# Optimization experiments

Measured on AMD Instinct MI355X. Metric: run time of the kernel, lower is better.

The kernel has to match this reference:

```python
import jax, jax.numpy as jnp
import numpy as np

# ---- static config mirroring __init__ kwargs ----
B, GH, GW = 64, 52, 52
A, NC = 5, 80            # anchor_number, class_number
HW = GH * GW
MAXB = 30                # max_box_per_image
NET_W, NET_H = 416.0, 416.0
COORD_SCALE, NOOBJ_SCALE, OBJ_SCALE, CLASS_SCALE = 5.0, 1.0, 5.0, 1.0
OBJ_THRESH = 0.5
ANCHORS_NP = np.array([[10., 14.], [23., 27.], [37., 58.], [81., 82.], [135., 169.]], dtype=np.float32)


def setup_inputs() -> dict:
    key = jax.random.key(0)
    k1, k2, k3, k4, k5, k6, k7, k8 = jax.random.split(key, 8)
    net_out = jax.random.normal(k1, (B, GH, GW, A * (NC + 5)), jnp.float32) * 0.5
    # encoded targets [B, A, 6, HW]: (x_off, y_off, w_log, h_log, conf, class)
    xy = jax.random.uniform(k2, (B, A, 2, HW), jnp.float32)
    whlog = jax.random.normal(k3, (B, A, 2, HW), jnp.float32) * 0.3
    conf = jax.random.uniform(k4, (B, A, 1, HW), jnp.float32)
    cls = jnp.floor(jax.random.uniform(k5, (B, A, 1, HW), jnp.float32) * NC)
    targets = jnp.concatenate([xy, whlog, conf, cls], axis=2)
    anchor_mask = (jax.random.uniform(k6, (B, A, HW), jnp.float32) < 0.02).astype(jnp.float32)
    # GT boxes (x1,y1,x2,y2) in image pixels
    ctr = jax.random.uniform(k7, (B, MAXB, 2), jnp.float32) * NET_W
    sz = jax.random.uniform(k8, (B, MAXB, 2), jnp.float32) * 100.0 + 10.0
    true_bboxs = jnp.concatenate([ctr - sz / 2, ctr + sz / 2], axis=-1)
    anchors = jnp.asarray(ANCHORS_NP)
    return {"net_out": net_out, "targets": targets, "anchor_mask": anchor_mask,
            "true_bboxs": true_bboxs, "anchors": anchors}


def _focal(p, t, gamma=2.0):
    # F.binary_cross_entropy elementwise, then focal modulation
    bce = -(t * jnp.log(p) + (1.0 - t) * jnp.log1p(-p))
    pt = jnp.exp(-bce)
    return (1.0 - pt) ** gamma * bce


def reference(net_out, targets, anchor_mask, true_bboxs, anchors):
    Bs, gh, gw, _ = net_out.shape
    hw = gh * gw
    x = net_out.reshape(Bs, A, NC + 5, hw)
    xy = jax.nn.sigmoid(x[:, :, :2, :])          # [B,A,2,HW]
    wh = x[:, :, 2:4, :]                          # raw w,h logits
    p_conf = jax.nn.sigmoid(x[:, :, 4, :])       # [B,A,HW]

    # ----- class loss (CE over positives) -----
    clas = x[:, :, 5:, :].reshape(Bs * A, NC, hw).transpose(0, 2, 1).reshape(-1, NC)
    clas_mask = anchor_mask.reshape(Bs * A, 1, hw).transpose(0, 2, 1).reshape(-1)
    t_clas = targets[:, :, 5, :].reshape(Bs * A, 1, hw).transpose(0, 2, 1).reshape(-1).astype(jnp.int32)
    logp = jax.nn.log_softmax(clas, axis=-1)
    clas_loss = (-jnp.take_along_axis(logp, t_clas[:, None], axis=1)[:, 0]) * clas_mask

    # ----- coordinate loss (masked, size-weighted MSE) -----
    am = anchor_mask[:, :, None, :]  # [B,A,1,HW]
    wh_scale = 2.0 - targets[:, :, 2:3, :] * targets[:, :, 3:4, :] / (NET_W * NET_H)
    xy_loss = (xy - targets[:, :, 0:2, :]) ** 2 * am * wh_scale
    wh_loss = (wh - targets[:, :, 2:4, :]) ** 2 * am * wh_scale
    coords_loss = xy_loss.sum() + wh_loss.sum()

    # ----- rescale predictions to image-space corner boxes -----
    col = jnp.tile(jnp.arange(gw), gh).astype(jnp.float32)      # [HW]
    row = jnp.repeat(jnp.arange(gh), gw).astype(jnp.float32)    # [HW] (square grid)
    aw = anchors[:, 0][None, :, None]
    ah = anchors[:, 1][None, :, None]
    px = (xy[:, :, 0, :] + col) / gw * NET_W
    py = (xy[:, :, 1, :] + row) / gh * NET_H
    pw = jnp.exp(wh[:, :, 0, :]) * aw
    ph = jnp.exp(wh[:, :, 1, :]) * ah
    x1 = px - pw / 2
    y1 = py - ph / 2
    pred = jnp.stack([x1, y1, x1 + pw, y1 + ph], axis=-1)       # [B,A,HW,4]
    pred = pred.transpose(0, 2, 1, 3)[:, :, :, None, :]         # [B,HW,A,1,4]

    # ----- broadcast IoU vs GT boxes -----
    tb = true_bboxs[:, None, None, :, :]                         # [B,1,1,M,4]
    tl = jnp.maximum(pred[..., :2], tb[..., :2])
    br = jnp.minimum(pred[..., 2:], tb[..., 2:])
    whi = jnp.maximum(br - tl, 0.0)
    inter = whi[..., 0] * whi[..., 1]
    a1 = (pred[..., 2] - pred[..., 0]) * (pred[..., 3] - pred[..., 1])
    a2 = (tb[..., 2] - tb[..., 0]) * (tb[..., 3] - tb[..., 1])
    iou = inter / (a1 + a2 - inter + 1e-5)                       # [B,HW,A,M]
    iou_max = iou.max(axis=-1)                                   # [B,HW,A]

    noobj_mask = 1.0 - anchor_mask
    label_noobj = (iou_max < OBJ_THRESH).astype(jnp.float32).transpose(0, 2, 1) * noobj_mask

    # ----- focal confidence losses -----
    t_conf = targets[:, :, 4, :]
    fl = _focal(p_conf, t_conf)
    obj_conf_loss = (anchor_mask * fl).sum()
    noobj_conf_loss = (label_noobj * fl).sum()

    total = (clas_loss.sum() * CLASS_SCALE
             + coords_loss * COORD_SCALE
             + obj_conf_loss * OBJ_SCALE
             + noobj_conf_loss * NOOBJ_SCALE) / Bs
    return total
```

## Files before the change

kernel.cpp:

```cpp
#include <hip/hip_runtime.h>

#define BATCH   64
#define GH      52
#define GWID    52
#define HW      2704
#define NA      5
#define NC      80
#define MAXB    30
#define CH_STRIDE HW
#define A_STRIDE  (85*HW)
#define B_STRIDE  (NA*85*HW)

__global__ __launch_bounds__(256) void yolo_main(
    const float* __restrict__ net_out,
    const float* __restrict__ targets,
    const float* __restrict__ amask,
    const float* __restrict__ tboxes,
    const float* __restrict__ anchors,
    float* __restrict__ partial)
{
    __shared__ float tb[MAXB * 4];
    __shared__ float wred[4];

    const int ba  = blockIdx.y;
    const int b   = ba / NA;
    const int a   = ba - b * NA;
    const int tid = threadIdx.x;

    if (tid < MAXB * 4) tb[tid] = tboxes[(size_t)b * (MAXB * 4) + tid];
    __syncthreads();

    const int p = blockIdx.x * 256 + tid;
    float local = 0.f;

    if (p < HW) {
        const size_t nb    = (size_t)b * B_STRIDE + (size_t)a * A_STRIDE + p;
        const size_t tbase = ((size_t)(b * NA + a) * 6) * HW + p;

        const float t_x   = targets[tbase];
        const float t_y   = targets[tbase + 1 * HW];
        const float t_w   = targets[tbase + 2 * HW];
        const float t_h   = targets[tbase + 3 * HW];
        const float t_c   = targets[tbase + 4 * HW];
        const int   t_cls = (int)targets[tbase + 5 * HW];

        const float am = amask[(size_t)(b * NA + a) * HW + p];

        const float zx = net_out[nb];
        const float zy = net_out[nb + 1 * CH_STRIDE];
        const float tw = net_out[nb + 2 * CH_STRIDE];
        const float th = net_out[nb + 3 * CH_STRIDE];
        const float zc = net_out[nb + 4 * CH_STRIDE];

        const float sx = 1.f / (1.f + __builtin_expf(-zx));
        const float sy = 1.f / (1.f + __builtin_expf(-zy));
        const float pc = 1.f / (1.f + __builtin_expf(-zc));

        const float ws = 2.f - t_w * t_h * (1.f / (416.f * 416.f));
        const float dx = sx - t_x, dy = sy - t_y, dw = tw - t_w, dh = th - t_h;
        const float coords = (dx * dx + dy * dy + dw * dw + dh * dh) * ws * am;

        const float log_pc   = -__builtin_logf(1.f + __builtin_expf(-zc));
        const float log_1mpc = -__builtin_logf(1.f + __builtin_expf(zc));
        const float bce = -(t_c * log_pc + (1.f - t_c) * log_1mpc);
        const float pt  = __builtin_expf(-bce);
        const float omp = 1.f - pt;
        const float fl  = omp * omp * bce;

        const float aw = anchors[a * 2 + 0];
        const float ah = anchors[a * 2 + 1];
        const float px = (sx + (float)(p % GWID)) * (416.f / (float)GWID);
        const float py = (sy + (float)(p / GWID)) * (416.f / (float)GH);
        const float pw = __builtin_expf(tw) * aw;
        const float ph = __builtin_expf(th) * ah;
        const float x1 = px - pw * 0.5f;
        const float y1 = py - ph * 0.5f;
        const float x2 = x1 + pw;
        const float y2 = y1 + ph;
        const float a1 = (x2 - x1) * (y2 - y1);

        float ioumax = 0.f;
        #pragma unroll
        for (int k = 0; k < MAXB; ++k) {
            const float bx1 = tb[k * 4 + 0];
            const float by1 = tb[k * 4 + 1];
            const float bx2 = tb[k * 4 + 2];
            const float by2 = tb[k * 4 + 3];
            const float tlx = fmaxf(x1, bx1);
            const float tly = fmaxf(y1, by1);
            const float brx = fminf(x2, bx2);
            const float bry = fminf(y2, by2);
            const float wi  = fmaxf(brx - tlx, 0.f);
            const float hi  = fmaxf(bry - tly, 0.f);
            const float inter = wi * hi;
            const float a2  = (bx2 - bx1) * (by2 - by1);
            const float iou = inter / (a1 + a2 - inter + 1e-5f);
            ioumax = fmaxf(ioumax, iou);
        }

        const float noobj = (ioumax < 0.5f) ? (1.f - am) : 0.f;

        local = 5.0f * coords + 5.0f * am * fl + noobj * fl;

        if (am > 0.f) {
            float lg[NC];
            #pragma unroll
            for (int c = 0; c < NC; ++c)
                lg[c] = net_out[nb + (size_t)(5 + c) * CH_STRIDE];
            float m = lg[0];
            #pragma unroll
            for (int c = 1; c < NC; ++c) m = fmaxf(m, lg[c]);
            float s = 0.f;
            #pragma unroll
            for (int c = 0; c < NC; ++c) s += __builtin_expf(lg[c] - m);
            float vt = 0.f;
            #pragma unroll
            for (int c = 0; c < NC; ++c) vt = (c == t_cls) ? lg[c] : vt;
            local += -(vt - m - __builtin_logf(s)) * am;
        }
    }

    #pragma unroll
    for (int off = 32; off > 0; off >>= 1)
        local += __shfl_down(local, off, 64);
    const int wid  = tid >> 6;
    const int lane = tid & 63;
    if (lane == 0) wred[wid] = local;
    __syncthreads();
    if (tid == 0) {
        partial[(size_t)blockIdx.y * gridDim.x + blockIdx.x] =
            wred[0] + wred[1] + wred[2] + wred[3];
    }
}

__global__ __launch_bounds__(256) void yolo_reduce(
    const float* __restrict__ partial, int n, float* __restrict__ out)
{
    __shared__ double sred[4];
    const int tid = threadIdx.x;
    double s = 0.0;
    for (int i = tid; i < n; i += 256) s += (double)partial[i];
    #pragma unroll
    for (int off = 32; off > 0; off >>= 1)
        s += __shfl_down(s, off, 64);
    const int wid  = tid >> 6;
    const int lane = tid & 63;
    if (lane == 0) sred[wid] = s;
    __syncthreads();
    if (tid == 0) {
        const double tot = sred[0] + sred[1] + sred[2] + sred[3];
        out[0] = (float)(tot / (double)BATCH);
    }
}

extern "C" void kernel_launch(void* const* d_in, const int* in_sizes, int n_in,
                              void* d_out, int out_size, void* d_ws, size_t ws_size,
                              hipStream_t stream) {
    const float* net_out = (const float*)d_in[0];
    const float* targets = (const float*)d_in[1];
    const float* amask   = (const float*)d_in[2];
    const float* tboxes  = (const float*)d_in[3];
    const float* anchors = (const float*)d_in[4];
    float* partial = (float*)d_ws;
    float* out = (float*)d_out;

    const int gx = (HW + 255) / 256;
    dim3 grid(gx, BATCH * NA);
    yolo_main<<<grid, 256, 0, stream>>>(net_out, targets, amask, tboxes, anchors, partial);
    yolo_reduce<<<1, 256, 0, stream>>>(partial, gx * BATCH * NA, out);
}
```

Baseline: 405.2 us.

## Compute class cross-entropy cooperatively across the wavefront per positive anchor

Positive anchors are found with a wavefront ballot, and each is handled by all 64 lanes. Each lane loads one or two class logits, and the max and sum-exp are done with xor shuffles, replacing the per-thread serial 80-element gather and loop. This removes divergent, strided per-thread loads and the large register array that could limit occupancy. Out-of-range threads are clamped to a valid pixel instead of branching, so uniform control flow can run the ballot loop. The cost is a serial loop over positives in each wave, with shuffle overhead per positive.

```diff
diff --git a/kernel.cpp b/kernel.cpp
--- a/kernel.cpp
+++ b/kernel.cpp
@@ -26,105 +26,120 @@
     const int b   = ba / NA;
     const int a   = ba - b * NA;
     const int tid = threadIdx.x;
+    const int lane = tid & 63;
 
     if (tid < MAXB * 4) tb[tid] = tboxes[(size_t)b * (MAXB * 4) + tid];
     __syncthreads();
 
-    const int p = blockIdx.x * 256 + tid;
-    float local = 0.f;
+    const int  p_raw = blockIdx.x * 256 + tid;
+    const bool valid = (p_raw < HW);
+    const int  p     = valid ? p_raw : (HW - 1);
 
-    if (p < HW) {
-        const size_t nb    = (size_t)b * B_STRIDE + (size_t)a * A_STRIDE + p;
-        const size_t tbase = ((size_t)(b * NA + a) * 6) * HW + p;
+    const size_t nbase = (size_t)b * B_STRIDE + (size_t)a * A_STRIDE;
+    const size_t nb    = nbase + p;
+    const size_t tbase = ((size_t)ba * 6) * HW + p;
 
-        const float t_x   = targets[tbase];
-        const float t_y   = targets[tbase + 1 * HW];
-        const float t_w   = targets[tbase + 2 * HW];
-        const float t_h   = targets[tbase + 3 * HW];
-        const float t_c   = targets[tbase + 4 * HW];
-        const int   t_cls = (int)targets[tbase + 5 * HW];
+    const float t_x   = targets[tbase];
+    const float t_y   = targets[tbase + 1 * HW];
+    const float t_w   = targets[tbase + 2 * HW];
+    const float t_h   = targets[tbase + 3 * HW];
+    const float t_c   = targets[tbase + 4 * HW];
+    const int   t_cls = (int)targets[tbase + 5 * HW];
 
-        const float am = amask[(size_t)(b * NA + a) * HW + p];
+    float am = amask[(size_t)ba * HW + p];
+    if (!valid) am = 0.f;
 
-        const float zx = net_out[nb];
-        const float zy = net_out[nb + 1 * CH_STRIDE];
-        const float tw = net_out[nb + 2 * CH_STRIDE];
-        const float th = net_out[nb + 3 * CH_STRIDE];
-        const float zc = net_out[nb + 4 * CH_STRIDE];
+    const float zx = net_out[nb];
+    const float zy = net_out[nb + 1 * CH_STRIDE];
+    const float tw = net_out[nb + 2 * CH_STRIDE];
+    const float th = net_out[nb + 3 * CH_STRIDE];
+    const float zc = net_out[nb + 4 * CH_STRIDE];
 
-        const float sx = 1.f / (1.f + __builtin_expf(-zx));
-        const float sy = 1.f / (1.f + __builtin_expf(-zy));
-        const float pc = 1.f / (1.f + __builtin_expf(-zc));
+    const float sx = 1.f / (1.f + __builtin_expf(-zx));
+    const float sy = 1.f / (1.f + __builtin_expf(-zy));
 
-        const float ws = 2.f - t_w * t_h * (1.f / (416.f * 416.f));
-        const float dx = sx - t_x, dy = sy - t_y, dw = tw - t_w, dh = th - t_h;
-        const float coords = (dx * dx + dy * dy + dw * dw + dh * dh) * ws * am;
+    const float ws = 2.f - t_w * t_h * (1.f / (416.f * 416.f));
+    const float dx = sx - t_x, dy = sy - t_y, dw = tw - t_w, dh = th - t_h;
+    const float coords = (dx * dx + dy * dy + dw * dw + dh * dh) * ws * am;
 
-        const float log_pc   = -__builtin_logf(1.f + __builtin_expf(-zc));
-        const float log_1mpc = -__builtin_logf(1.f + __builtin_expf(zc));
-        const float bce = -(t_c * log_pc + (1.f - t_c) * log_1mpc);
-        const float pt  = __builtin_expf(-bce);
-        const float omp = 1.f - pt;
-        const float fl  = omp * omp * bce;
+    const float log_pc   = -__builtin_logf(1.f + __builtin_expf(-zc));
+    const float log_1mpc = -__builtin_logf(1.f + __builtin_expf(zc));
+    const float bce = -(t_c * log_pc + (1.f - t_c) * log_1mpc);
+    const float pt  = __builtin_expf(-bce);
+    const float omp = 1.f - pt;
+    const float fl  = omp * omp * bce;
 
-        const float aw = anchors[a * 2 + 0];
-        const float ah = anchors[a * 2 + 1];
-        const float px = (sx + (float)(p % GWID)) * (416.f / (float)GWID);
-        const float py = (sy + (float)(p / GWID)) * (416.f / (float)GH);
-        const float pw = __builtin_expf(tw) * aw;
-        const float ph = __builtin_expf(th) * ah;
-        const float x1 = px - pw * 0.5f;
-        const float y1 = py - ph * 0.5f;
-        const float x2 = x1 + pw;
-        const float y2 = y1 + ph;
-        const float a1 = (x2 - x1) * (y2 - y1);
+    const float aw = anchors[a * 2 + 0];
+    const float ah = anchors[a * 2 + 1];
+    const float px = (sx + (float)(p % GWID)) * (416.f / (float)GWID);
+    const float py = (sy + (float)(p / GWID)) * (416.f / (float)GH);
+    const float pw = __builtin_expf(tw) * aw;
+    const float ph = __builtin_expf(th) * ah;
+    const float x1 = px - pw * 0.5f;
+    const float y1 = py - ph * 0.5f;
+    const float x2 = x1 + pw;
+    const float y2 = y1 + ph;
+    const float a1 = (x2 - x1) * (y2 - y1);
 
-        float ioumax = 0.f;
+    float ioumax = 0.f;
+    #pragma unroll
+    for (int k = 0; k < MAXB; ++k) {
+        const float bx1 = tb[k * 4 + 0];
+        const float by1 = tb[k * 4 + 1];
+        const float bx2 = tb[k * 4 + 2];
+        const float by2 = tb[k * 4 + 3];
+        const float tlx = fmaxf(x1, bx1);
+        const float tly = fmaxf(y1, by1);
+        const float brx = fminf(x2, bx2);
+        const float bry = fminf(y2, by2);
+        const float wi  = fmaxf(brx - tlx, 0.f);
+        const float hi  = fmaxf(bry - tly, 0.f);
+        const float inter = wi * hi;
+        const float a2  = (bx2 - bx1) * (by2 - by1);
+        const float iou = inter / (a1 + a2 - inter + 1e-5f);
+        ioumax = fmaxf(ioumax, iou);
+    }
+
+    const float noobj = (ioumax < 0.5f) ? (1.f - am) : 0.f;
+
+    float local = valid ? (5.0f * coords + 5.0f * am * fl + noobj * fl) : 0.f;
+
+    unsigned long long mb = __ballot(am > 0.f);
+    while (mb) {
+        const int src = __ffsll((long long)mb) - 1;
+        mb &= mb - 1;
+        const int   p_s  = __shfl(p, src, 64);
+        const float am_s = __shfl(am, src, 64);
+        const int   tc_s = __shfl(t_cls, src, 64);
+
+        const size_t cb = nbase + (size_t)5 * CH_STRIDE + p_s;
+        const float v0 = net_out[cb + (size_t)lane * CH_STRIDE];
+        const float v1 = (lane < NC - 64)
+                       ? net_out[cb + (size_t)(64 + lane) * CH_STRIDE]
+                       : -1e30f;
+
+        float mx = fmaxf(v0, v1);
         #pragma unroll
-        for (int k = 0; k < MAXB; ++k) {
-            const float bx1 = tb[k * 4 + 0];
-            const float by1 = tb[k * 4 + 1];
-            const float bx2 = tb[k * 4 + 2];
-            const float by2 = tb[k * 4 + 3];
-            const float tlx = fmaxf(x1, bx1);
-            const float tly = fmaxf(y1, by1);
-            const float brx = fminf(x2, bx2);
-            const float bry = fminf(y2, by2);
-            const float wi  = fmaxf(brx - tlx, 0.f);
-            const float hi  = fmaxf(bry - tly, 0.f);
-            const float inter = wi * hi;
-            const float a2  = (bx2 - bx1) * (by2 - by1);
-            const float iou = inter / (a1 + a2 - inter + 1e-5f);
-            ioumax = fmaxf(ioumax, iou);
-        }
+        for (int off = 32; off > 0; off >>= 1)
+            mx = fmaxf(mx, __shfl_xor(mx, off, 64));
 
-        const float noobj = (ioumax < 0.5f) ? (1.f - am) : 0.f;
+        float e = __builtin_expf(v0 - mx)
+                + ((lane < NC - 64) ? __builtin_expf(v1 - mx) : 0.f);
+        #pragma unroll
+        for (int off = 32; off > 0; off >>= 1)
+            e += __shfl_xor(e, off, 64);
 
-        local = 5.0f * coords + 5.0f * am * fl + noobj * fl;
+        const float vt = (tc_s < 64) ? __shfl(v0, tc_s, 64)
+                                     : __shfl(v1, tc_s - 64, 64);
 
-        if (am > 0.f) {
-            float lg[NC];
-            #pragma unroll
-            for (int c = 0; c < NC; ++c)
-                lg[c] = net_out[nb + (size_t)(5 + c) * CH_STRIDE];
-            float m = lg[0];
-            #pragma unroll
-            for (int c = 1; c < NC; ++c) m = fmaxf(m, lg[c]);
-            float s = 0.f;
-            #pragma unroll
-            for (int c = 0; c < NC; ++c) s += __builtin_expf(lg[c] - m);
-            float vt = 0.f;
-            #pragma unroll
-            for (int c = 0; c < NC; ++c) vt = (c == t_cls) ? lg[c] : vt;
-            local += -(vt - m - __builtin_logf(s)) * am;
-        }
+        if ((int)lane == src)
+            local += -(vt - mx - __builtin_logf(e)) * am_s;
     }
 
     #pragma unroll
     for (int off = 32; off > 0; off >>= 1)
         local += __shfl_down(local, off, 64);
-    const int wid  = tid >> 6;
-    const int lane = tid & 63;
+    const int wid = tid >> 6;
     if (lane == 0) wred[wid] = local;
     __syncthreads();
     if (tid == 0) {
```

Result: faster. 385.0 us (-5.0%).

## Split class loss into compacted positive-list kernel with wave-per-anchor softmax

Applied to the files above, without the earlier changes.

The dense kernel now handles four pixels per thread with float4 loads and reuses each shared-memory GT box across those four IoU evaluations. Positive anchors are compacted into a global descriptor list with ballot and atomicAdd, so they no longer make whole waves diverge. A second kernel computes the 80-class cross-entropy for each positive with one wave per anchor and shuffle reductions. This adds a memset, an extra launch and an atomic counter, and the summation order of the final result changes.

```diff
diff --git a/kernel.cpp b/kernel.cpp
--- a/kernel.cpp
+++ b/kernel.cpp
@@ -9,137 +9,219 @@
 #define MAXB    30
 #define CH_STRIDE HW
 #define A_STRIDE  (85*HW)
-#define B_STRIDE  (NA*85*HW)
-
-__global__ __launch_bounds__(256) void yolo_main(
+#define NBA       (BATCH*NA)
+
+#define WS_PARTA   1024
+#define WS_PARTB   8192
+#define WS_DESC    16384
+#define WS_AMV     (16384 + (4<<20))
+
+#define GX_DENSE   3
+#define GB_CLASS   2048
+
+__global__ __launch_bounds__(256) void yolo_dense(
     const float* __restrict__ net_out,
     const float* __restrict__ targets,
     const float* __restrict__ amask,
     const float* __restrict__ tboxes,
     const float* __restrict__ anchors,
-    float* __restrict__ partial)
+    unsigned*    __restrict__ counter,
+    float*       __restrict__ partialA,
+    unsigned*    __restrict__ desc,
+    float*       __restrict__ amv)
 {
     __shared__ float tb[MAXB * 4];
     __shared__ float wred[4];
 
-    const int ba  = blockIdx.y;
-    const int b   = ba / NA;
-    const int a   = ba - b * NA;
-    const int tid = threadIdx.x;
+    const int ba   = blockIdx.y;
+    const int b    = ba / NA;
+    const int a    = ba - b * NA;
+    const int tid  = threadIdx.x;
+    const int lane = tid & 63;
 
     if (tid < MAXB * 4) tb[tid] = tboxes[(size_t)b * (MAXB * 4) + tid];
     __syncthreads();
 
-    const int p = blockIdx.x * 256 + tid;
-    float local = 0.f;
-
-    if (p < HW) {
-        const size_t nb    = (size_t)b * B_STRIDE + (size_t)a * A_STRIDE + p;
-        const size_t tbase = ((size_t)(b * NA + a) * 6) * HW + p;
-
-        const float t_x   = targets[tbase];
-        const float t_y   = targets[tbase + 1 * HW];
-        const float t_w   = targets[tbase + 2 * HW];
-        const float t_h   = targets[tbase + 3 * HW];
-        const float t_c   = targets[tbase + 4 * HW];
-        const int   t_cls = (int)targets[tbase + 5 * HW];
-
-        const float am = amask[(size_t)(b * NA + a) * HW + p];
-
-        const float zx = net_out[nb];
-        const float zy = net_out[nb + 1 * CH_STRIDE];
-        const float tw = net_out[nb + 2 * CH_STRIDE];
-        const float th = net_out[nb + 3 * CH_STRIDE];
-        const float zc = net_out[nb + 4 * CH_STRIDE];
-
-        const float sx = 1.f / (1.f + __builtin_expf(-zx));
-        const float sy = 1.f / (1.f + __builtin_expf(-zy));
-        const float pc = 1.f / (1.f + __builtin_expf(-zc));
-
-        const float ws = 2.f - t_w * t_h * (1.f / (416.f * 416.f));
-        const float dx = sx - t_x, dy = sy - t_y, dw = tw - t_w, dh = th - t_h;
-        const float coords = (dx * dx + dy * dy + dw * dw + dh * dh) * ws * am;
-
-        const float log_pc   = -__builtin_logf(1.f + __builtin_expf(-zc));
-        const float log_1mpc = -__builtin_logf(1.f + __builtin_expf(zc));
-        const float bce = -(t_c * log_pc + (1.f - t_c) * log_1mpc);
-        const float pt  = __builtin_expf(-bce);
-        const float omp = 1.f - pt;
-        const float fl  = omp * omp * bce;
-
-        const float aw = anchors[a * 2 + 0];
-        const float ah = anchors[a * 2 + 1];
-        const float px = (sx + (float)(p % GWID)) * (416.f / (float)GWID);
-        const float py = (sy + (float)(p / GWID)) * (416.f / (float)GH);
-        const float pw = __builtin_expf(tw) * aw;
-        const float ph = __builtin_expf(th) * ah;
-        const float x1 = px - pw * 0.5f;
-        const float y1 = py - ph * 0.5f;
-        const float x2 = x1 + pw;
-        const float y2 = y1 + ph;
-        const float a1 = (x2 - x1) * (y2 - y1);
-
-        float ioumax = 0.f;
-        #pragma unroll
-        for (int k = 0; k < MAXB; ++k) {
-            const float bx1 = tb[k * 4 + 0];
-            const float by1 = tb[k * 4 + 1];
-            const float bx2 = tb[k * 4 + 2];
-            const float by2 = tb[k * 4 + 3];
-            const float tlx = fmaxf(x1, bx1);
-            const float tly = fmaxf(y1, by1);
-            const float brx = fminf(x2, bx2);
-            const float bry = fminf(y2, by2);
-            const float wi  = fmaxf(brx - tlx, 0.f);
-            const float hi  = fmaxf(bry - tly, 0.f);
+    const int  p0    = (blockIdx.x * 256 + tid) * 4;
+    const bool valid = (p0 < HW);
+    const size_t nb    = (size_t)ba * A_STRIDE + (valid ? p0 : 0);
+    const size_t tbase = (size_t)ba * 6 * HW   + (valid ? p0 : 0);
+
+    float zx[4], zy[4], twp[4], thp[4], zc[4];
+    float t_x[4], t_y[4], t_w[4], t_h[4], t_c[4], tcl[4], am[4];
+
+    if (valid) {
+        float4 v;
+        v = *(const float4*)(net_out + nb);                 zx[0]=v.x; zx[1]=v.y; zx[2]=v.z; zx[3]=v.w;
+        v = *(const float4*)(net_out + nb + 1*CH_STRIDE);   zy[0]=v.x; zy[1]=v.y; zy[2]=v.z; zy[3]=v.w;
+        v = *(const float4*)(net_out + nb + 2*CH_STRIDE);   twp[0]=v.x;twp[1]=v.y;twp[2]=v.z;twp[3]=v.w;
+        v = *(const float4*)(net_out + nb + 3*CH_STRIDE);   thp[0]=v.x;thp[1]=v.y;thp[2]=v.z;thp[3]=v.w;
+        v = *(const float4*)(net_out + nb + 4*CH_STRIDE);   zc[0]=v.x; zc[1]=v.y; zc[2]=v.z; zc[3]=v.w;
+        v = *(const float4*)(targets + tbase);              t_x[0]=v.x;t_x[1]=v.y;t_x[2]=v.z;t_x[3]=v.w;
+        v = *(const float4*)(targets + tbase + 1*HW);       t_y[0]=v.x;t_y[1]=v.y;t_y[2]=v.z;t_y[3]=v.w;
+        v = *(const float4*)(targets + tbase + 2*HW);       t_w[0]=v.x;t_w[1]=v.y;t_w[2]=v.z;t_w[3]=v.w;
+        v = *(const float4*)(targets + tbase + 3*HW);       t_h[0]=v.x;t_h[1]=v.y;t_h[2]=v.z;t_h[3]=v.w;
+        v = *(const float4*)(targets + tbase + 4*HW);       t_c[0]=v.x;t_c[1]=v.y;t_c[2]=v.z;t_c[3]=v.w;
+        v = *(const float4*)(targets + tbase + 5*HW);       tcl[0]=v.x;tcl[1]=v.y;tcl[2]=v.z;tcl[3]=v.w;
+        v = *(const float4*)(amask + (size_t)ba * HW + p0); am[0]=v.x; am[1]=v.y; am[2]=v.z; am[3]=v.w;
+    } else {
+        #pragma unroll
+        for (int j = 0; j < 4; ++j) {
+            zx[j]=zy[j]=twp[j]=thp[j]=zc[j]=0.f;
+            t_x[j]=t_y[j]=t_w[j]=t_h[j]=t_c[j]=tcl[j]=am[j]=0.f;
+        }
+    }
+
+    const float aw = anchors[a * 2 + 0];
+    const float ah = anchors[a * 2 + 1];
+
+    float sx[4], sy[4], x1[4], y1[4], x2[4], y2[4], a1[4], io[4];
+    #pragma unroll
+    for (int j = 0; j < 4; ++j) {
+        sx[j] = 1.f / (1.f + __builtin_expf(-zx[j]));
+        sy[j] = 1.f / (1.f + __builtin_expf(-zy[j]));
+        const int p = p0 + j;
+        const float px = (sx[j] + (float)(p % GWID)) * (416.f / (float)GWID);
+        const float py = (sy[j] + (float)(p / GWID)) * (416.f / (float)GH);
+        const float pw = __builtin_expf(twp[j]) * aw;
+        const float ph = __builtin_expf(thp[j]) * ah;
+        x1[j] = px - pw * 0.5f;
+        y1[j] = py - ph * 0.5f;
+        x2[j] = x1[j] + pw;
+        y2[j] = y1[j] + ph;
+        a1[j] = pw * ph;
+        io[j] = 0.f;
+    }
+
+    #pragma unroll
+    for (int k = 0; k < MAXB; ++k) {
+        const float bx1 = tb[k * 4 + 0];
+        const float by1 = tb[k * 4 + 1];
+        const float bx2 = tb[k * 4 + 2];
+        const float by2 = tb[k * 4 + 3];
+        const float a2  = (bx2 - bx1) * (by2 - by1);
+        #pragma unroll
+        for (int j = 0; j < 4; ++j) {
+            const float wi = fmaxf(fminf(x2[j], bx2) - fmaxf(x1[j], bx1), 0.f);
+            const float hi = fmaxf(fminf(y2[j], by2) - fmaxf(y1[j], by1), 0.f);
             const float inter = wi * hi;
-            const float a2  = (bx2 - bx1) * (by2 - by1);
-            const float iou = inter / (a1 + a2 - inter + 1e-5f);
-            ioumax = fmaxf(ioumax, iou);
-        }
-
-        const float noobj = (ioumax < 0.5f) ? (1.f - am) : 0.f;
-
-        local = 5.0f * coords + 5.0f * am * fl + noobj * fl;
-
-        if (am > 0.f) {
-            float lg[NC];
-            #pragma unroll
-            for (int c = 0; c < NC; ++c)
-                lg[c] = net_out[nb + (size_t)(5 + c) * CH_STRIDE];
-            float m = lg[0];
-            #pragma unroll
-            for (int c = 1; c < NC; ++c) m = fmaxf(m, lg[c]);
-            float s = 0.f;
-            #pragma unroll
-            for (int c = 0; c < NC; ++c) s += __builtin_expf(lg[c] - m);
-            float vt = 0.f;
-            #pragma unroll
-            for (int c = 0; c < NC; ++c) vt = (c == t_cls) ? lg[c] : vt;
-            local += -(vt - m - __builtin_logf(s)) * am;
+            const float iou = inter / (a1[j] + a2 - inter + 1e-5f);
+            io[j] = fmaxf(io[j], iou);
+        }
+    }
+
+    float lsum = 0.f;
+    if (valid) {
+        #pragma unroll
+        for (int j = 0; j < 4; ++j) {
+            const float ws = 2.f - t_w[j] * t_h[j] * (1.f / (416.f * 416.f));
+            const float dx = sx[j] - t_x[j], dy = sy[j] - t_y[j];
+            const float dw = twp[j] - t_w[j], dh = thp[j] - t_h[j];
+            const float coords = (dx*dx + dy*dy + dw*dw + dh*dh) * ws * am[j];
+
+            const float log_pc   = -__builtin_logf(1.f + __builtin_expf(-zc[j]));
+            const float log_1mpc = -__builtin_logf(1.f + __builtin_expf(zc[j]));
+            const float bce = -(t_c[j] * log_pc + (1.f - t_c[j]) * log_1mpc);
+            const float pt  = __builtin_expf(-bce);
+            const float omp = 1.f - pt;
+            const float fl  = omp * omp * bce;
+
+            const float noobj = (io[j] < 0.5f) ? (1.f - am[j]) : 0.f;
+            lsum += 5.0f * coords + 5.0f * am[j] * fl + noobj * fl;
+        }
+    }
+
+    #pragma unroll
+    for (int j = 0; j < 4; ++j) {
+        const bool m = (am[j] > 0.f);
+        const unsigned long long msk = __ballot(m);
+        if (msk) {
+            unsigned base = 0;
+            if (lane == 0) base = atomicAdd(counter, (unsigned)__popcll(msk));
+            base = (unsigned)__shfl((int)base, 0, 64);
+            if (m) {
+                const int rank = __popcll(msk & ((1ull << lane) - 1ull));
+                const int p = p0 + j;
+                desc[base + rank] = (unsigned)p | ((unsigned)ba << 12)
+                                  | ((unsigned)(int)tcl[j] << 21);
+                amv[base + rank] = am[j];
+            }
         }
     }
 
     #pragma unroll
     for (int off = 32; off > 0; off >>= 1)
-        local += __shfl_down(local, off, 64);
+        lsum += __shfl_down(lsum, off, 64);
+    const int wid = tid >> 6;
+    if (lane == 0) wred[wid] = lsum;
+    __syncthreads();
+    if (tid == 0)
+        partialA[(size_t)blockIdx.y * GX_DENSE + blockIdx.x] =
+            wred[0] + wred[1] + wred[2] + wred[3];
+}
+
+__global__ __launch_bounds__(256) void yolo_class(
+    const float*    __restrict__ net_out,
+    const unsigned* __restrict__ counter,
+    const unsigned* __restrict__ desc,
+    const float*    __restrict__ amv,
+    float*          __restrict__ partialB)
+{
+    __shared__ float w4[4];
+    const int tid  = threadIdx.x;
+    const int lane = tid & 63;
     const int wid  = tid >> 6;
-    const int lane = tid & 63;
-    if (lane == 0) wred[wid] = local;
-    __syncthreads();
-    if (tid == 0) {
-        partial[(size_t)blockIdx.y * gridDim.x + blockIdx.x] =
-            wred[0] + wred[1] + wred[2] + wred[3];
-    }
-}
-
-__global__ __launch_bounds__(256) void yolo_reduce(
-    const float* __restrict__ partial, int n, float* __restrict__ out)
+    const int gwave  = blockIdx.x * 4 + wid;
+    const int nwaves = gridDim.x * 4;
+    const int count  = (int)*counter;
+
+    float acc = 0.f;
+    for (int i = gwave; i < count; i += nwaves) {
+        const unsigned d   = desc[i];
+        const float amv_i  = amv[i];
+        const int p    = d & 0xFFF;
+        const int bav  = (d >> 12) & 0x1FF;
+        const int tcls = (int)(d >> 21);
+        const size_t cb = (size_t)bav * A_STRIDE + (size_t)5 * HW + p;
+
+        const float v0 = net_out[cb + (size_t)lane * HW];
+        const float v1 = (lane < (NC - 64))
+                       ? net_out[cb + (size_t)(64 + lane) * HW]
+                       : -1e30f;
+
+        float mx = fmaxf(v0, v1);
+        #pragma unroll
+        for (int off = 32; off > 0; off >>= 1)
+            mx = fmaxf(mx, __shfl_xor(mx, off, 64));
+
+        float e = __builtin_expf(v0 - mx)
+                + ((lane < (NC - 64)) ? __builtin_expf(v1 - mx) : 0.f);
+        #pragma unroll
+        for (int off = 32; off > 0; off >>= 1)
+            e += __shfl_xor(e, off, 64);
+
+        const float vt = (tcls < 64) ? __shfl(v0, tcls, 64)
+                                     : __shfl(v1, tcls - 64, 64);
+
+        if (lane == 0)
+            acc += -(vt - mx - __builtin_logf(e)) * amv_i;
+    }
+
+    if (lane == 0) w4[wid] = acc;
+    __syncthreads();
+    if (tid == 0) partialB[blockIdx.x] = w4[0] + w4[1] + w4[2] + w4[3];
+}
+
+__global__ __launch_bounds__(256) void yolo_final(
+    const float* __restrict__ partialA, int nA,
+    const float* __restrict__ partialB, int nB,
+    float* __restrict__ out)
 {
     __shared__ double sred[4];
     const int tid = threadIdx.x;
     double s = 0.0;
-    for (int i = tid; i < n; i += 256) s += (double)partial[i];
+    for (int i = tid; i < nA; i += 256) s += (double)partialA[i];
+    for (int i = tid; i < nB; i += 256) s += (double)partialB[i];
     #pragma unroll
     for (int off = 32; off > 0; off >>= 1)
         s += __shfl_down(s, off, 64);
@@ -161,11 +243,20 @@
     const float* amask   = (const float*)d_in[2];
     const float* tboxes  = (const float*)d_in[3];
     const float* anchors = (const float*)d_in[4];
-    float* partial = (float*)d_ws;
-    float* out = (float*)d_out;
-
-    const int gx = (HW + 255) / 256;
-    dim3 grid(gx, BATCH * NA);
-    yolo_main<<<grid, 256, 0, stream>>>(net_out, targets, amask, tboxes, anchors, partial);
-    yolo_reduce<<<1, 256, 0, stream>>>(partial, gx * BATCH * NA, out);
-}
+
+    char* ws = (char*)d_ws;
+    unsigned* counter  = (unsigned*)ws;
+    float*    partialA = (float*)(ws + WS_PARTA);
+    float*    partialB = (float*)(ws + WS_PARTB);
+    unsigned* desc     = (unsigned*)(ws + WS_DESC);
+    float*    amv      = (float*)(ws + WS_AMV);
+    float*    out      = (float*)d_out;
+
+    hipMemsetAsync(counter, 0, 64, stream);
+
+    dim3 gridA(GX_DENSE, NBA);
+    yolo_dense<<<gridA, 256, 0, stream>>>(net_out, targets, amask, tboxes, anchors,
+                                          counter, partialA, desc, amv);
+    yolo_class<<<GB_CLASS, 256, 0, stream>>>(net_out, counter, desc, amv, partialB);
+    yolo_final<<<1, 256, 0, stream>>>(partialA, GX_DENSE * NBA, partialB, GB_CLASS, out);
+}
```

New measurement: 501.3 us. 1.24x slower.
